# Optimization experiments

Hardware: AMD Instinct MI355X
Metric: run time of the kernel (lower is better)

## Reference

```python
import jax, jax.numpy as jnp
import numpy as np

B, N, VD, ED, HD, V, T = 64, 196, 512, 512, 512, 10000, 20


def setup_inputs() -> dict:
    key = jax.random.key(0)
    ks = jax.random.split(key, 12)
    s = lambda k, shape: jax.random.normal(k, shape, jnp.float32) * 0.02
    return {
        "features": jax.random.normal(ks[0], (B, N, VD), jnp.float32),
        "captions": jax.random.randint(ks[1], (B, T), 0, V),
        "W_init_h": s(ks[2], (HD, VD)),
        "W_init_c": s(ks[3], (HD, VD)),
        "W_av": s(ks[4], (1, VD)),
        "b_av": jnp.zeros((1,), jnp.float32),
        "W_ah": s(ks[5], (1, HD)),
        "b_ah": jnp.zeros((1,), jnp.float32),
        "embed": s(ks[6], (V, ED)),
        "W_ih": s(ks[7], (4 * HD, VD + ED)),
        "W_hh": s(ks[8], (4 * HD, HD)),
        "b_ih": jnp.zeros((4 * HD,), jnp.float32),
        "b_hh": jnp.zeros((4 * HD,), jnp.float32),
        "W_out": s(ks[9], (V, HD)),
        "b_out": jnp.zeros((V,), jnp.float32),
    }


def reference(features, captions, W_init_h, W_init_c, W_av, b_av, W_ah, b_ah,
              embed, W_ih, W_hh, b_ih, b_hh, W_out, b_out):
    vis_num = features.shape[1]
    # init hidden/cell: sum over vis_num of Linear(features) / vis_num
    h0 = jnp.einsum('bnv,hv->bh', features, W_init_h) / vis_num  # [B,H]
    c0 = jnp.einsum('bnv,hv->bh', features, W_init_c) / vis_num  # [B,H]
    # word embeddings, time-major: [T,B,E]
    emb = jnp.swapaxes(embed[captions], 0, 1)
    # visual part of additive attention is step-invariant: precompute [B,N,1]
    att_v = jnp.einsum('bnv,ov->bno', features, W_av) + b_av

    def step(carry, e_t):
        h, c = carry
        att_h = h @ W_ah.T + b_ah                          # [B,1]
        attn = jax.nn.softmax(att_v + att_h[:, None, :], axis=1)  # [B,N,1]
        ctx = jnp.sum(features * attn, axis=1)             # [B,VD]
        x = jnp.concatenate([ctx, e_t], axis=1)            # [B,VD+ED]
        gates = x @ W_ih.T + b_ih + h @ W_hh.T + b_hh      # [B,4H]
        i, f, g, o = jnp.split(gates, 4, axis=1)
        c = jax.nn.sigmoid(f) * c + jax.nn.sigmoid(i) * jnp.tanh(g)
        h = jax.nn.sigmoid(o) * jnp.tanh(c)
        words = h @ W_out.T + b_out                        # [B,V]
        return (h, c), words

    _, word_space = jax.lax.scan(step, (h0, c0), emb)      # [T,B,V]
    return jax.nn.log_softmax(word_space, axis=2), jax.nn.softmax(word_space, axis=2)
```

## Files before the change

kernel.cpp:

```cpp
#include <hip/hip_runtime.h>
#include <math.h>

#define B_   64
#define N_   196
#define VD_  512
#define ED_  512
#define HD_  512
#define V_   10000
#define T_   20
#define G4_  2048
#define LSTM_NBLK 32

typedef __attribute__((ext_vector_type(8))) short bf16x8;
typedef __attribute__((ext_vector_type(4))) float f32x4;

static __device__ __forceinline__ float sigmoidf_(float x) {
  return 1.f / (1.f + __expf(-x));
}

static __device__ __forceinline__ float tanh_fast(float x) {
  float e = __expf(2.f * x);
  return 1.f - 2.f / (e + 1.f);
}

static __device__ __forceinline__ unsigned short f2bf_(float x) {
  unsigned u = __float_as_uint(x);
  unsigned r = (u + 0x7FFFu + ((u >> 16) & 1u)) >> 16;
  return (unsigned short)r;
}

__global__ void k_prep(const float* __restrict__ W_out,
                       const float* __restrict__ W_ih,
                       const float* __restrict__ W_hh,
                       const float* __restrict__ embed,
                       const int* __restrict__ caps,
                       const float* __restrict__ feat,
                       const float* __restrict__ W_av,
                       unsigned short* __restrict__ wout_bf,
                       unsigned short* __restrict__ wihe_bf,
                       unsigned short* __restrict__ whh_bf,
                       unsigned short* __restrict__ emb_bf,
                       float* __restrict__ svg) {
  int bx = blockIdx.x, tid = threadIdx.x;
  if (bx >= 7688) {
    int r = bx - 7688;
    int b = r >> 2, q = r & 3;
    int lane = tid & 63, w = tid >> 6;
    const float* fb = feat + (size_t)b * (N_ * VD_);
    float4 wv0 = *(const float4*)(W_av + lane * 8);
    float4 wv1 = *(const float4*)(W_av + lane * 8 + 4);
    int nbase = q * 49;
    for (int n = nbase + w; n < nbase + 49; n += 4) {
      const float* fp = fb + n * VD_ + lane * 8;
      float4 f0 = *(const float4*)fp;
      float4 f1 = *(const float4*)(fp + 4);
      float p = f0.x * wv0.x + f0.y * wv0.y + f0.z * wv0.z + f0.w * wv0.w
              + f1.x * wv1.x + f1.y * wv1.y + f1.z * wv1.z + f1.w * wv1.w;
#pragma unroll
      for (int off = 32; off > 0; off >>= 1) p += __shfl_down(p, off, 64);
      if (lane == 0) svg[b * N_ + n] = p;
    }
    return;
  }
  float4 v; unsigned short* dst; int i;
  if (bx < 5000) {
    i = bx * 256 + tid;
    v = ((const float4*)W_out)[i];
    dst = wout_bf;
  } else if (bx < 6024) {
    i = (bx - 5000) * 256 + tid;
    int j = i >> 7, kk = (i & 127) << 2;
    v = *(const float4*)(W_ih + (size_t)j * (VD_ + ED_) + VD_ + kk);
    dst = wihe_bf;
  } else if (bx < 6664) {
    i = (bx - 6024) * 256 + tid;
    int row = i >> 7;
    int b = row & 63, t = row >> 6;
    v = *(const float4*)(embed + (size_t)caps[b * T_ + t] * ED_ + ((i & 127) << 2));
    dst = emb_bf;
  } else {
    i = (bx - 6664) * 256 + tid;
    v = ((const float4*)W_hh)[i];
    dst = whh_bf;
  }
  ushort4 o;
  o.x = f2bf_(v.x); o.y = f2bf_(v.y); o.z = f2bf_(v.z); o.w = f2bf_(v.w);
  ((ushort4*)dst)[i] = o;
}

__global__ void k_attn2(const float* __restrict__ feat,
                        const float* __restrict__ svg,
                        float* __restrict__ fmean,
                        float* __restrict__ ctx) {
  __shared__ float sa[200];
  __shared__ float red[8];
  __shared__ float pc[2][128];
  __shared__ float pf[2][128];
  int b = blockIdx.x, q = blockIdx.y;
  int tid = threadIdx.x, lane = tid & 63, w = tid >> 6;
  const float* fb = feat + (size_t)b * (N_ * VD_);

  float v = (tid < N_) ? svg[b * N_ + tid] : -1e30f;
  float m = v;
#pragma unroll
  for (int off = 32; off > 0; off >>= 1) m = fmaxf(m, __shfl_down(m, off, 64));
  if (lane == 0) red[w] = m;
  __syncthreads();
  m = fmaxf(fmaxf(red[0], red[1]), fmaxf(red[2], red[3]));

  float e = (tid < N_) ? __expf(v - m) : 0.f;
  float s = e;
#pragma unroll
  for (int off = 32; off > 0; off >>= 1) s += __shfl_down(s, off, 64);
  if (lane == 0) red[4 + w] = s;
  __syncthreads();
  float inv = 1.f / (red[4] + red[5] + red[6] + red[7]);
  if (tid < N_) sa[tid] = e * inv;
  __syncthreads();

  int d = q * 128 + (tid & 127);
  int nh = tid >> 7;
  float c = 0.f, fs = 0.f;
  for (int n = nh; n < N_; n += 2) {
    float f = fb[n * VD_ + d];
    c += sa[n] * f;
    fs += f;
  }
  pc[nh][tid & 127] = c;
  pf[nh][tid & 127] = fs;
  __syncthreads();
  if (tid < 128) {
    ctx[b * VD_ + q * 128 + tid] = pc[0][tid] + pc[1][tid];
    fmean[b * VD_ + q * 128 + tid] = (pf[0][tid] + pf[1][tid]) * (1.f / N_);
  }
}

#define BK 16
__global__ __launch_bounds__(256) void k_small(
    const float* __restrict__ fmean, const float* __restrict__ ctx,
    const float* __restrict__ W_init_h, const float* __restrict__ W_init_c,
    const float* __restrict__ W_ih,
    const float* __restrict__ b_ih, const float* __restrict__ b_hh,
    float* __restrict__ hbuf, float* __restrict__ cbuf, float* __restrict__ gctx,
    unsigned short* __restrict__ h0_bf) {
  const float* A; const float* Bw; float* C;
  int ldb, ldc, n0;
  const float* bias1 = nullptr; const float* bias2 = nullptr;
  unsigned short* hb = nullptr;
  int bx = blockIdx.x;
  if (bx < 8)       { A = fmean; Bw = W_init_h; C = hbuf; ldb = VD_; ldc = HD_; n0 = bx * 64; hb = h0_bf; }
  else if (bx < 16) { A = fmean; Bw = W_init_c; C = cbuf; ldb = VD_; ldc = HD_; n0 = (bx - 8) * 64; }
  else { A = ctx; Bw = W_ih; C = gctx; ldb = VD_ + ED_; ldc = G4_; n0 = (bx - 16) * 64;
         bias1 = b_ih; bias2 = b_hh; }

  __shared__ float As[BK][64];
  __shared__ float Bs[BK][64];
  int tid = threadIdx.x;
  int tm = tid & 15, tn = tid >> 4;
  int sr = tid >> 2, sk = (tid & 3) * 4;
  const float* arow = A + (size_t)sr * VD_;
  const float* brow = Bw + (size_t)(n0 + sr) * ldb;
  float acc[4][4] = {};

  for (int k0 = 0; k0 < VD_; k0 += BK) {
    float4 av = *(const float4*)(arow + k0 + sk);
    float4 bv = *(const float4*)(brow + k0 + sk);
    __syncthreads();
    As[sk + 0][sr] = av.x; As[sk + 1][sr] = av.y;
    As[sk + 2][sr] = av.z; As[sk + 3][sr] = av.w;
    Bs[sk + 0][sr] = bv.x; Bs[sk + 1][sr] = bv.y;
    Bs[sk + 2][sr] = bv.z; Bs[sk + 3][sr] = bv.w;
    __syncthreads();
#pragma unroll
    for (int kk = 0; kk < BK; ++kk) {
      float4 a4 = *(const float4*)&As[kk][tm * 4];
      float4 b4 = *(const float4*)&Bs[kk][tn * 4];
      acc[0][0] += a4.x * b4.x; acc[0][1] += a4.x * b4.y; acc[0][2] += a4.x * b4.z; acc[0][3] += a4.x * b4.w;
      acc[1][0] += a4.y * b4.x; acc[1][1] += a4.y * b4.y; acc[1][2] += a4.y * b4.z; acc[1][3] += a4.y * b4.w;
      acc[2][0] += a4.z * b4.x; acc[2][1] += a4.z * b4.y; acc[2][2] += a4.z * b4.z; acc[2][3] += a4.z * b4.w;
      acc[3][0] += a4.w * b4.x; acc[3][1] += a4.w * b4.y; acc[3][2] += a4.w * b4.z; acc[3][3] += a4.w * b4.w;
    }
  }
#pragma unroll
  for (int j = 0; j < 4; ++j) {
    int n = n0 + tn * 4 + j;
    float bb = (bias1 ? bias1[n] + bias2[n] : 0.f);
#pragma unroll
    for (int i = 0; i < 4; ++i) {
      int mm = tm * 4 + i;
      float val = acc[i][j] + bb;
      C[(size_t)mm * ldc + n] = val;
      if (hb) hb[(size_t)mm * HD_ + n] = f2bf_(val);
    }
  }
}

__global__ __launch_bounds__(256) void k_gemm_mfma(
    const unsigned short* __restrict__ A,
    const unsigned short* __restrict__ Bw,
    const float* __restrict__ bias,
    const float* __restrict__ radd, int ldr,
    float* __restrict__ C, int M, int Nn, int K) {
  __shared__ unsigned short As[128][32];
  __shared__ unsigned short Bs[128][32];
  int tid = threadIdx.x;
  int wave = tid >> 6, lane = tid & 63;
  int wm = wave & 1, wn = wave >> 1;
  int m0 = blockIdx.y * 128, n0 = blockIdx.x * 128;
  int l15 = lane & 15, quad = lane >> 4;
  int sr = tid >> 1, skq = (tid & 1) * 16;
  const unsigned short* ga = A + (size_t)(m0 + sr) * K + skq;
  int bn = n0 + sr; if (bn >= Nn) bn = Nn - 1;
  const unsigned short* gb = Bw + (size_t)bn * K + skq;

  f32x4 acc[4][4];
#pragma unroll
  for (int i = 0; i < 4; ++i)
#pragma unroll
    for (int j = 0; j < 4; ++j) acc[i][j] = (f32x4){0.f, 0.f, 0.f, 0.f};

  for (int k0 = 0; k0 < K; k0 += 32) {
    bf16x8 a0 = *(const bf16x8*)(ga + k0);
    bf16x8 a1 = *(const bf16x8*)(ga + k0 + 8);
    bf16x8 b0 = *(const bf16x8*)(gb + k0);
    bf16x8 b1 = *(const bf16x8*)(gb + k0 + 8);
    __syncthreads();
    *(bf16x8*)&As[sr][skq] = a0; *(bf16x8*)&As[sr][skq + 8] = a1;
    *(bf16x8*)&Bs[sr][skq] = b0; *(bf16x8*)&Bs[sr][skq + 8] = b1;
    __syncthreads();
    bf16x8 af[4], bfr[4];
#pragma unroll
    for (int mt = 0; mt < 4; ++mt)
      af[mt] = *(const bf16x8*)&As[wm * 64 + mt * 16 + l15][quad * 8];
#pragma unroll
    for (int nt = 0; nt < 4; ++nt)
      bfr[nt] = *(const bf16x8*)&Bs[wn * 64 + nt * 16 + l15][quad * 8];
#pragma unroll
    for (int mt = 0; mt < 4; ++mt)
#pragma unroll
      for (int nt = 0; nt < 4; ++nt)
        acc[mt][nt] = __builtin_amdgcn_mfma_f32_16x16x32_bf16(af[mt], bfr[nt], acc[mt][nt], 0, 0, 0);
  }

#pragma unroll
  for (int nt = 0; nt < 4; ++nt) {
    int n = n0 + wn * 64 + nt * 16 + l15;
    if (n < Nn) {
      float bb = bias ? bias[n] : 0.f;
#pragma unroll
      for (int mt = 0; mt < 4; ++mt) {
        int mbase = m0 + wm * 64 + mt * 16 + quad * 4;
#pragma unroll
        for (int r = 0; r < 4; ++r) {
          int mg = mbase + r;
          float ra = radd ? radd[(size_t)(mg & 63) * ldr + n] : 0.f;
          C[(size_t)mg * Nn + n] = acc[mt][nt][r] + bb + ra;
        }
      }
    }
  }
}

__global__ __launch_bounds__(256, 1) void k_lstm_mfma(
    const unsigned short* __restrict__ whh_bf,
    const float* __restrict__ gpre,
    const unsigned short* __restrict__ h0_bf,
    const float* __restrict__ c0,
    unsigned short* __restrict__ hall_bf,
    int* __restrict__ bar) {
  __shared__ unsigned short whh_s[64 * 512];
  int tid = threadIdx.x;
  int w = tid >> 6, lane = tid & 63;
  int l15 = lane & 15, quad = lane >> 4;
  int n0 = blockIdx.x * 16;

  for (int idx = tid; idx < 4096; idx += 256) {
    int r = idx >> 6, gg = idx & 63;
    int gate = r >> 4, l = r & 15;
    bf16x8 v = *(const bf16x8*)(whh_bf +
        (size_t)(gate * HD_ + n0 + l) * HD_ + gg * 8);
    *(bf16x8*)&whh_s[r * 512 + (gg ^ (r & 7)) * 8] = v;
  }

  int brow = w * 16 + quad * 4;

  float c_reg[4];
#pragma unroll
  for (int r = 0; r < 4; ++r)
    c_reg[r] = c0[(size_t)(brow + r) * HD_ + n0 + l15];

  float gr[16];
#pragma unroll
  for (int g = 0; g < 4; ++g)
#pragma unroll
    for (int r = 0; r < 4; ++r)
      gr[g * 4 + r] = gpre[(size_t)(brow + r) * G4_ + g * HD_ + n0 + l15];

  __syncthreads();

  for (int t = 0; t < T_; ++t) {
    const unsigned short* h_in =
        (t == 0) ? h0_bf : (hall_bf + (size_t)(t - 1) * B_ * HD_);
    const unsigned short* ar = h_in + (size_t)(w * 16 + l15) * HD_ + quad * 8;

    bf16x8 a[16];
#pragma unroll
    for (int ki = 0; ki < 16; ++ki)
      asm volatile("global_load_dwordx4 %0, %1, off sc0 sc1"
                   : "=v"(a[ki]) : "v"(ar + ki * 32) : "memory");
    asm volatile("s_waitcnt vmcnt(0)" ::: "memory");
    __builtin_amdgcn_sched_barrier(0);

    f32x4 acc[4];
#pragma unroll
    for (int i = 0; i < 4; ++i) acc[i] = (f32x4){0.f, 0.f, 0.f, 0.f};

#pragma unroll
    for (int ki = 0; ki < 16; ++ki) {
      int rb = l15 * 512 + (((ki * 4 + quad) ^ (l15 & 7)) << 3);
#pragma unroll
      for (int nt = 0; nt < 4; ++nt) {
        bf16x8 b = *(const bf16x8*)&whh_s[nt * 16 * 512 + rb];
        acc[nt] = __builtin_amdgcn_mfma_f32_16x16x32_bf16(a[ki], b, acc[nt], 0, 0, 0);
      }
    }

    unsigned short* hout = hall_bf + (size_t)t * B_ * HD_;
#pragma unroll
    for (int r = 0; r < 4; ++r) {
      float gi = acc[0][r] + gr[0 + r];
      float gf = acc[1][r] + gr[4 + r];
      float gg = acc[2][r] + gr[8 + r];
      float go = acc[3][r] + gr[12 + r];
      float cn = sigmoidf_(gf) * c_reg[r] + sigmoidf_(gi) * tanh_fast(gg);
      c_reg[r] = cn;
      unsigned hv = f2bf_(sigmoidf_(go) * tanh_fast(cn));
      unsigned short* sp = hout + (size_t)(brow + r) * HD_ + n0 + l15;
      asm volatile("global_store_short %0, %1, off sc0 sc1"
                   :: "v"(sp), "v"(hv) : "memory");
    }

    if (t < T_ - 1) {
      asm volatile("s_waitcnt vmcnt(0)" ::: "memory");
      __syncthreads();
      if (tid == 0) {
        int* fp = bar + blockIdx.x * 16;
        int fv = t + 1;
        asm volatile("global_store_dword %0, %1, off sc0 sc1"
                     :: "v"(fp), "v"(fv) : "memory");
      }
      const float* gpt = gpre + (size_t)(t + 1) * B_ * G4_;
#pragma unroll
      for (int g = 0; g < 4; ++g)
#pragma unroll
        for (int r = 0; r < 4; ++r)
          gr[g * 4 + r] = gpt[(size_t)(brow + r) * G4_ + g * HD_ + n0 + l15];
      if (tid < 64) {
        int* fp = bar + (tid & 31) * 16;
        while (true) {
          int v = __hip_atomic_load(fp, __ATOMIC_RELAXED,
                                    __HIP_MEMORY_SCOPE_AGENT);
          if (__all(v >= t + 1)) break;
          __builtin_amdgcn_s_sleep(1);
        }
      }
      __syncthreads();
    }
  }
}

__global__ void k_softmax(float* __restrict__ logits, float* __restrict__ out1) {
  __shared__ float red[8];
  int row = blockIdx.x, tid = threadIdx.x;
  int lane = tid & 63, wid = tid >> 6;
  float* lr = logits + (size_t)row * V_;
  float* o1 = out1 + (size_t)row * V_;
  const int NV4 = V_ / 4;

  float m = -1e30f;
  for (int i = tid; i < NV4; i += 256) {
    float4 v = ((const float4*)lr)[i];
    m = fmaxf(m, fmaxf(fmaxf(v.x, v.y), fmaxf(v.z, v.w)));
  }
#pragma unroll
  for (int off = 32; off > 0; off >>= 1) m = fmaxf(m, __shfl_down(m, off, 64));
  if (lane == 0) red[4 + wid] = m;
  __syncthreads();
  m = fmaxf(fmaxf(red[4], red[5]), fmaxf(red[6], red[7]));

  float s = 0.f;
  for (int i = tid; i < NV4; i += 256) {
    float4 v = ((const float4*)lr)[i];
    s += __expf(v.x - m) + __expf(v.y - m) + __expf(v.z - m) + __expf(v.w - m);
  }
#pragma unroll
  for (int off = 32; off > 0; off >>= 1) s += __shfl_down(s, off, 64);
  if (lane == 0) red[wid] = s;
  __syncthreads();
  s = red[0] + red[1] + red[2] + red[3];
  float ls = __logf(s), inv = 1.f / s;

  for (int i = tid; i < NV4; i += 256) {
    float4 v = ((const float4*)lr)[i];
    float4 a, bb;
    a.x = v.x - m - ls; a.y = v.y - m - ls; a.z = v.z - m - ls; a.w = v.w - m - ls;
    bb.x = __expf(v.x - m) * inv; bb.y = __expf(v.y - m) * inv;
    bb.z = __expf(v.z - m) * inv; bb.w = __expf(v.w - m) * inv;
    ((float4*)o1)[i] = a;
    ((float4*)lr)[i] = bb;
  }
}

extern "C" void kernel_launch(void* const* d_in, const int* in_sizes, int n_in,
                              void* d_out, int out_size, void* d_ws, size_t ws_size,
                              hipStream_t stream) {
  const float* features = (const float*)d_in[0];
  const int*   captions = (const int*)d_in[1];
  const float* W_init_h = (const float*)d_in[2];
  const float* W_init_c = (const float*)d_in[3];
  const float* W_av     = (const float*)d_in[4];
  const float* embed    = (const float*)d_in[8];
  const float* W_ih     = (const float*)d_in[9];
  const float* W_hh     = (const float*)d_in[10];
  const float* b_ih     = (const float*)d_in[11];
  const float* b_hh     = (const float*)d_in[12];
  const float* W_out    = (const float*)d_in[13];
  const float* b_out    = (const float*)d_in[14];

  float* ws    = (float*)d_ws;
  float* fmean = ws;
  float* ctx   = fmean + B_ * VD_;
  float* hbuf  = ctx + B_ * VD_;
  float* cbuf  = hbuf + B_ * HD_;
  float* gctx  = cbuf + B_ * HD_;
  float* svg   = gctx + (size_t)B_ * G4_;
  float* gpre  = svg + 12608;
  int*   bar   = (int*)(gpre + (size_t)T_ * B_ * G4_);
  unsigned short* wout_bf = (unsigned short*)(bar + 512);
  unsigned short* wihe_bf = wout_bf + (size_t)V_ * HD_;
  unsigned short* whh_bf  = wihe_bf + (size_t)G4_ * ED_;
  unsigned short* emb_bf  = whh_bf + (size_t)G4_ * HD_;
  unsigned short* h0_bf   = emb_bf + (size_t)T_ * B_ * ED_;
  unsigned short* hall_bf = h0_bf + (size_t)B_ * HD_;

  float* out1   = (float*)d_out;
  float* logits = out1 + (size_t)T_ * B_ * V_;

  hipMemsetAsync(bar, 0, 2048, stream);

  k_prep<<<7944, 256, 0, stream>>>(W_out, W_ih, W_hh, embed, captions,
                                   features, W_av,
                                   wout_bf, wihe_bf, whh_bf, emb_bf, svg);
  k_attn2<<<dim3(B_, 4), 256, 0, stream>>>(features, svg, fmean, ctx);
  k_small<<<48, 256, 0, stream>>>(fmean, ctx, W_init_h, W_init_c, W_ih,
                                  b_ih, b_hh, hbuf, cbuf, gctx, h0_bf);

  k_gemm_mfma<<<dim3(G4_ / 128, (T_ * B_) / 128), 256, 0, stream>>>(
      emb_bf, wihe_bf, nullptr, gctx, G4_, gpre, T_ * B_, G4_, ED_);

  k_lstm_mfma<<<LSTM_NBLK, 256, 0, stream>>>(
      whh_bf, gpre, h0_bf, cbuf, hall_bf, bar);

  k_gemm_mfma<<<dim3((V_ + 127) / 128, (T_ * B_) / 128), 256, 0, stream>>>(
      hall_bf, wout_bf, b_out, nullptr, 0, logits, T_ * B_, V_, HD_);

  k_softmax<<<T_ * B_, 256, 0, stream>>>(logits, out1);
}
```

Baseline: 469.6 us.

## Fuse LSTM recurrence with output-projection GEMM using flag-based producer/consumer overlap

```diff
diff --git a/kernel.cpp b/kernel.cpp
--- a/kernel.cpp
+++ b/kernel.cpp
@@ -10,6 +10,8 @@
 #define T_   20
 #define G4_  2048
 #define LSTM_NBLK 32
+#define WNW   224
+#define NITEM 790
 
 typedef __attribute__((ext_vector_type(8))) short bf16x8;
 typedef __attribute__((ext_vector_type(4))) float f32x4;
@@ -261,110 +263,196 @@
   }
 }
 
-__global__ __launch_bounds__(256, 1) void k_lstm_mfma(
+__global__ __launch_bounds__(256, 1) void k_lstm_logits(
     const unsigned short* __restrict__ whh_bf,
     const float* __restrict__ gpre,
     const unsigned short* __restrict__ h0_bf,
     const float* __restrict__ c0,
     unsigned short* __restrict__ hall_bf,
-    int* __restrict__ bar) {
-  __shared__ unsigned short whh_s[64 * 512];
+    int* __restrict__ bar,
+    const unsigned short* __restrict__ wout_bf,
+    const float* __restrict__ b_out,
+    float* __restrict__ logits) {
+  __shared__ unsigned short smem[64 * 512];
+  int bx = blockIdx.x;
   int tid = threadIdx.x;
-  int w = tid >> 6, lane = tid & 63;
+  int wave = tid >> 6, lane = tid & 63;
   int l15 = lane & 15, quad = lane >> 4;
-  int n0 = blockIdx.x * 16;
-
-  for (int idx = tid; idx < 4096; idx += 256) {
-    int r = idx >> 6, gg = idx & 63;
-    int gate = r >> 4, l = r & 15;
-    bf16x8 v = *(const bf16x8*)(whh_bf +
-        (size_t)(gate * HD_ + n0 + l) * HD_ + gg * 8);
-    *(bf16x8*)&whh_s[r * 512 + (gg ^ (r & 7)) * 8] = v;
-  }
-
-  int brow = w * 16 + quad * 4;
-
-  float c_reg[4];
-#pragma unroll
-  for (int r = 0; r < 4; ++r)
-    c_reg[r] = c0[(size_t)(brow + r) * HD_ + n0 + l15];
-
-  float gr[16];
-#pragma unroll
-  for (int g = 0; g < 4; ++g)
+
+  if (bx < LSTM_NBLK) {
+    int w = wave;
+    int n0 = bx * 16;
+
+    for (int idx = tid; idx < 4096; idx += 256) {
+      int r = idx >> 6, gg = idx & 63;
+      int gate = r >> 4, l = r & 15;
+      bf16x8 v = *(const bf16x8*)(whh_bf +
+          (size_t)(gate * HD_ + n0 + l) * HD_ + gg * 8);
+      *(bf16x8*)&smem[r * 512 + (gg ^ (r & 7)) * 8] = v;
+    }
+
+    int brow = w * 16 + quad * 4;
+
+    float c_reg[4];
 #pragma unroll
     for (int r = 0; r < 4; ++r)
-      gr[g * 4 + r] = gpre[(size_t)(brow + r) * G4_ + g * HD_ + n0 + l15];
-
-  __syncthreads();
-
-  for (int t = 0; t < T_; ++t) {
-    const unsigned short* h_in =
-        (t == 0) ? h0_bf : (hall_bf + (size_t)(t - 1) * B_ * HD_);
-    const unsigned short* ar = h_in + (size_t)(w * 16 + l15) * HD_ + quad * 8;
-
-    bf16x8 a[16];
-#pragma unroll
-    for (int ki = 0; ki < 16; ++ki)
-      asm volatile("global_load_dwordx4 %0, %1, off sc0 sc1"
-                   : "=v"(a[ki]) : "v"(ar + ki * 32) : "memory");
-    asm volatile("s_waitcnt vmcnt(0)" ::: "memory");
-    __builtin_amdgcn_sched_barrier(0);
-
-    f32x4 acc[4];
-#pragma unroll
-    for (int i = 0; i < 4; ++i) acc[i] = (f32x4){0.f, 0.f, 0.f, 0.f};
-
-#pragma unroll
-    for (int ki = 0; ki < 16; ++ki) {
-      int rb = l15 * 512 + (((ki * 4 + quad) ^ (l15 & 7)) << 3);
-#pragma unroll
-      for (int nt = 0; nt < 4; ++nt) {
-        bf16x8 b = *(const bf16x8*)&whh_s[nt * 16 * 512 + rb];
-        acc[nt] = __builtin_amdgcn_mfma_f32_16x16x32_bf16(a[ki], b, acc[nt], 0, 0, 0);
-      }
-    }
-
-    unsigned short* hout = hall_bf + (size_t)t * B_ * HD_;
-#pragma unroll
-    for (int r = 0; r < 4; ++r) {
-      float gi = acc[0][r] + gr[0 + r];
-      float gf = acc[1][r] + gr[4 + r];
-      float gg = acc[2][r] + gr[8 + r];
-      float go = acc[3][r] + gr[12 + r];
-      float cn = sigmoidf_(gf) * c_reg[r] + sigmoidf_(gi) * tanh_fast(gg);
-      c_reg[r] = cn;
-      unsigned hv = f2bf_(sigmoidf_(go) * tanh_fast(cn));
-      unsigned short* sp = hout + (size_t)(brow + r) * HD_ + n0 + l15;
-      asm volatile("global_store_short %0, %1, off sc0 sc1"
-                   :: "v"(sp), "v"(hv) : "memory");
-    }
-
-    if (t < T_ - 1) {
+      c_reg[r] = c0[(size_t)(brow + r) * HD_ + n0 + l15];
+
+    float gr[16];
+#pragma unroll
+    for (int g = 0; g < 4; ++g)
+#pragma unroll
+      for (int r = 0; r < 4; ++r)
+        gr[g * 4 + r] = gpre[(size_t)(brow + r) * G4_ + g * HD_ + n0 + l15];
+
+    __syncthreads();
+
+    for (int t = 0; t < T_; ++t) {
+      const unsigned short* h_in =
+          (t == 0) ? h0_bf : (hall_bf + (size_t)(t - 1) * B_ * HD_);
+      const unsigned short* ar = h_in + (size_t)(w * 16 + l15) * HD_ + quad * 8;
+
+      bf16x8 a[16];
+#pragma unroll
+      for (int ki = 0; ki < 16; ++ki)
+        asm volatile("global_load_dwordx4 %0, %1, off sc0 sc1"
+                     : "=v"(a[ki]) : "v"(ar + ki * 32) : "memory");
+      asm volatile("s_waitcnt vmcnt(0)" ::: "memory");
+      __builtin_amdgcn_sched_barrier(0);
+
+      f32x4 acc[4];
+#pragma unroll
+      for (int i = 0; i < 4; ++i) acc[i] = (f32x4){0.f, 0.f, 0.f, 0.f};
+
+#pragma unroll
+      for (int ki = 0; ki < 16; ++ki) {
+        int rb = l15 * 512 + (((ki * 4 + quad) ^ (l15 & 7)) << 3);
+#pragma unroll
+        for (int nt = 0; nt < 4; ++nt) {
+          bf16x8 b = *(const bf16x8*)&smem[nt * 16 * 512 + rb];
+          acc[nt] = __builtin_amdgcn_mfma_f32_16x16x32_bf16(a[ki], b, acc[nt], 0, 0, 0);
+        }
+      }
+
+      unsigned short* hout = hall_bf + (size_t)t * B_ * HD_;
+#pragma unroll
+      for (int r = 0; r < 4; ++r) {
+        float gi = acc[0][r] + gr[0 + r];
+        float gf = acc[1][r] + gr[4 + r];
+        float gg = acc[2][r] + gr[8 + r];
+        float go = acc[3][r] + gr[12 + r];
+        float cn = sigmoidf_(gf) * c_reg[r] + sigmoidf_(gi) * tanh_fast(gg);
+        c_reg[r] = cn;
+        unsigned hv = f2bf_(sigmoidf_(go) * tanh_fast(cn));
+        unsigned short* sp = hout + (size_t)(brow + r) * HD_ + n0 + l15;
+        asm volatile("global_store_short %0, %1, off sc0 sc1"
+                     :: "v"(sp), "v"(hv) : "memory");
+      }
+
       asm volatile("s_waitcnt vmcnt(0)" ::: "memory");
       __syncthreads();
       if (tid == 0) {
-        int* fp = bar + blockIdx.x * 16;
+        int* fp = bar + bx * 16;
         int fv = t + 1;
         asm volatile("global_store_dword %0, %1, off sc0 sc1"
                      :: "v"(fp), "v"(fv) : "memory");
       }
-      const float* gpt = gpre + (size_t)(t + 1) * B_ * G4_;
-#pragma unroll
-      for (int g = 0; g < 4; ++g)
-#pragma unroll
-        for (int r = 0; r < 4; ++r)
-          gr[g * 4 + r] = gpt[(size_t)(brow + r) * G4_ + g * HD_ + n0 + l15];
+      if (t < T_ - 1) {
+        const float* gpt = gpre + (size_t)(t + 1) * B_ * G4_;
+#pragma unroll
+        for (int g = 0; g < 4; ++g)
+#pragma unroll
+          for (int r = 0; r < 4; ++r)
+            gr[g * 4 + r] = gpt[(size_t)(brow + r) * G4_ + g * HD_ + n0 + l15];
+        if (tid < 64) {
+          int* fp = bar + (tid & 31) * 16;
+          while (true) {
+            int v = __hip_atomic_load(fp, __ATOMIC_RELAXED,
+                                      __HIP_MEMORY_SCOPE_AGENT);
+            if (__all(v >= t + 1)) break;
+            __builtin_amdgcn_s_sleep(1);
+          }
+        }
+        __syncthreads();
+      }
+    }
+  } else {
+    int wq = bx - LSTM_NBLK;
+    unsigned short (*As)[32] = (unsigned short (*)[32])smem;
+    unsigned short (*Bs)[32] = (unsigned short (*)[32])(smem + 128 * 32);
+    int wm = wave & 1, wn = wave >> 1;
+    int sr = tid >> 1, skq = (tid & 1) * 16;
+
+    for (int q = wq; q < NITEM; q += WNW) {
+      int mt_ = q / 79, vt = q - mt_ * 79;
+      int m0 = mt_ * 128, n0 = vt * 128;
+      int tneed = (m0 >> 6) + 2;
+
       if (tid < 64) {
-        int* fp = bar + (tid & 31) * 16;
+        const int* fp = bar + (tid & 31) * 16;
         while (true) {
           int v = __hip_atomic_load(fp, __ATOMIC_RELAXED,
                                     __HIP_MEMORY_SCOPE_AGENT);
-          if (__all(v >= t + 1)) break;
-          __builtin_amdgcn_s_sleep(1);
+          if (__all(v >= tneed)) break;
+          __builtin_amdgcn_s_sleep(16);
         }
       }
       __syncthreads();
+
+      const unsigned short* ga = hall_bf + (size_t)(m0 + sr) * HD_ + skq;
+      int bn = n0 + sr; if (bn >= V_) bn = V_ - 1;
+      const unsigned short* gb = wout_bf + (size_t)bn * HD_ + skq;
+
+      f32x4 acc[4][4];
+#pragma unroll
+      for (int i = 0; i < 4; ++i)
+#pragma unroll
+        for (int j = 0; j < 4; ++j) acc[i][j] = (f32x4){0.f, 0.f, 0.f, 0.f};
+
+      for (int k0 = 0; k0 < HD_; k0 += 32) {
+        bf16x8 a0, a1, b0v, b1v;
+        asm volatile("global_load_dwordx4 %0, %1, off sc0 sc1"
+                     : "=v"(a0) : "v"(ga + k0) : "memory");
+        asm volatile("global_load_dwordx4 %0, %1, off sc0 sc1"
+                     : "=v"(a1) : "v"(ga + k0 + 8) : "memory");
+        b0v = *(const bf16x8*)(gb + k0);
+        b1v = *(const bf16x8*)(gb + k0 + 8);
+        asm volatile("s_waitcnt vmcnt(0)" ::: "memory");
+        __syncthreads();
+        *(bf16x8*)&As[sr][skq] = a0; *(bf16x8*)&As[sr][skq + 8] = a1;
+        *(bf16x8*)&Bs[sr][skq] = b0v; *(bf16x8*)&Bs[sr][skq + 8] = b1v;
+        __syncthreads();
+        bf16x8 af[4], bfr[4];
+#pragma unroll
+        for (int mt = 0; mt < 4; ++mt)
+          af[mt] = *(const bf16x8*)&As[wm * 64 + mt * 16 + l15][quad * 8];
+#pragma unroll
+        for (int nt = 0; nt < 4; ++nt)
+          bfr[nt] = *(const bf16x8*)&Bs[wn * 64 + nt * 16 + l15][quad * 8];
+#pragma unroll
+        for (int mt = 0; mt < 4; ++mt)
+#pragma unroll
+          for (int nt = 0; nt < 4; ++nt)
+            acc[mt][nt] = __builtin_amdgcn_mfma_f32_16x16x32_bf16(
+                af[mt], bfr[nt], acc[mt][nt], 0, 0, 0);
+      }
+
+#pragma unroll
+      for (int nt = 0; nt < 4; ++nt) {
+        int n = n0 + wn * 64 + nt * 16 + l15;
+        if (n < V_) {
+          float bb = b_out[n];
+#pragma unroll
+          for (int mt = 0; mt < 4; ++mt) {
+            int mbase = m0 + wm * 64 + mt * 16 + quad * 4;
+#pragma unroll
+            for (int r = 0; r < 4; ++r) {
+              int mg = mbase + r;
+              logits[(size_t)mg * V_ + n] = acc[mt][nt][r] + bb;
+            }
+          }
+        }
+      }
     }
   }
 }
@@ -458,11 +546,8 @@
   k_gemm_mfma<<<dim3(G4_ / 128, (T_ * B_) / 128), 256, 0, stream>>>(
       emb_bf, wihe_bf, nullptr, gctx, G4_, gpre, T_ * B_, G4_, ED_);
 
-  k_lstm_mfma<<<LSTM_NBLK, 256, 0, stream>>>(
-      whh_bf, gpre, h0_bf, cbuf, hall_bf, bar);
-
-  k_gemm_mfma<<<dim3((V_ + 127) / 128, (T_ * B_) / 128), 256, 0, stream>>>(
-      hall_bf, wout_bf, b_out, nullptr, 0, logits, T_ * B_, V_, HD_);
+  k_lstm_logits<<<LSTM_NBLK + WNW, 256, 0, stream>>>(
+      whh_bf, gpre, h0_bf, cbuf, hall_bf, bar, wout_bf, b_out, logits);
 
   k_softmax<<<T_ * B_, 256, 0, stream>>>(logits, out1);
 }
```

Result: faster. 442.4 us (-5.8%).
